# Kernel tuning notes

Measured on AMD Instinct MI355X. Metric: run time of the kernel, lower is better.

## Reference

```python
import jax, jax.numpy as jnp
import numpy as np

T, H, I, E, K, L, R = 1024, 1024, 1024, 8, 2, 4, 16
N = 2 * I  # gate_up dim


def setup_inputs() -> dict:
    key = jax.random.key(0)
    ks = jax.random.split(key, 12)
    tw = jax.random.uniform(ks[1], (T, K), dtype=jnp.float32) + 0.1
    tw = tw / tw.sum(axis=-1, keepdims=True)  # routing weights sum to 1
    return {
        "hidden_states": jax.random.normal(ks[0], (T, H), dtype=jnp.float32),
        "topk_weights": tw,
        "w13": jax.random.normal(ks[2], (E, N, H), dtype=jnp.float32) * (1.0 / np.sqrt(H)),
        "w2": jax.random.normal(ks[3], (E, H, I), dtype=jnp.float32) * (1.0 / np.sqrt(I)),
        "gate_up_lora_a": jax.random.normal(ks[4], (L, E, R, H), dtype=jnp.float32) * (1.0 / np.sqrt(H)),
        "gate_up_lora_b": jax.random.normal(ks[5], (L, E, N, R), dtype=jnp.float32) * (1.0 / np.sqrt(R)),
        "down_lora_a": jax.random.normal(ks[6], (L, E, R, I), dtype=jnp.float32) * (1.0 / np.sqrt(I)),
        "down_lora_b": jax.random.normal(ks[7], (L, E, H, R), dtype=jnp.float32) * (1.0 / np.sqrt(R)),
        "scalings": jax.random.uniform(ks[8], (L,), dtype=jnp.float32) + 0.5,
        "topk_ids": jax.random.randint(ks[9], (T, K), 0, E, dtype=jnp.int32),
        "lora_indices": jax.random.randint(ks[10], (T,), 0, L, dtype=jnp.int32),
    }


def reference(hidden_states, topk_weights, w13, w2, gate_up_lora_a,
              gate_up_lora_b, down_lora_a, down_lora_b, scalings,
              topk_ids, lora_indices):
    num_tokens, hidden = hidden_states.shape
    num_experts, gate_up_dim, _ = w13.shape
    top_k = topk_ids.shape[1]
    inter = gate_up_dim // 2
    TKp = num_tokens * top_k

    e_flat = topk_ids.reshape(-1)                      # [TK] expert per dispatched pair
    l_flat = jnp.repeat(lora_indices, top_k)           # [TK] adapter per pair
    w_flat = topk_weights.reshape(-1)                  # [TK] routing weight
    x_rep = jnp.repeat(hidden_states, top_k, axis=0)   # [TK, H]

    # ---- grouped gate_up GEMM (base path): cache1[p] = x[p] @ w13[e(p)]^T ----
    cache1 = jnp.zeros((TKp, gate_up_dim), dtype=hidden_states.dtype)
    for ei in range(num_experts):  # small fixed expert count
        mask = (e_flat == ei)[:, None]
        cache1 = cache1 + jnp.where(mask, x_rep @ w13[ei].T, 0.0)

    # ---- per-expert gate_up LoRA delta, injected BEFORE activation ----
    scal = scalings[l_flat][:, None]                   # [TK, 1]
    Ag = gate_up_lora_a[l_flat, e_flat]                # [TK, R, H]
    Bg = gate_up_lora_b[l_flat, e_flat]                # [TK, N, R]
    tmp = jnp.einsum('prh,ph->pr', Ag, x_rep)
    cache1 = cache1 + jnp.einsum('pnr,pr->pn', Bg, tmp) * scal

    # ---- silu_and_mul on (base + lora) ----
    act = jax.nn.silu(cache1[:, :inter]) * cache1[:, inter:]   # [TK, I]

    # ---- grouped down GEMM (base), routed-weight applied ----
    cache3 = jnp.zeros((TKp, hidden), dtype=hidden_states.dtype)
    for ei in range(num_experts):
        mask = (e_flat == ei)[:, None]
        cache3 = cache3 + jnp.where(mask, act @ w2[ei].T, 0.0)
    cache3 = cache3 * w_flat[:, None]

    # ---- per-expert down LoRA delta (weighted by routing weight) ----
    Ad = down_lora_a[l_flat, e_flat]                   # [TK, R, I]
    Bd = down_lora_b[l_flat, e_flat]                   # [TK, H, R]
    tmpd = jnp.einsum('pri,pi->pr', Ad, act)
    cache3 = cache3 + jnp.einsum('phr,pr->ph', Bd, tmpd) * scal * w_flat[:, None]

    # ---- combine expert outputs (moe_sum over top_k slots) ----
    return cache3.reshape(num_tokens, top_k, hidden).sum(axis=1)
```

## Files before the change

### kernel.cpp

```cpp
#include <hip/hip_runtime.h>
#include <stdint.h>

#define Td 1024
#define Hd 1024
#define Id 1024
#define Ed 8
#define Kd 2
#define Ld 4
#define Rd 16
#define Nd 2048
#define TKd (Td*Kd)

typedef __bf16 bf16x8 __attribute__((ext_vector_type(8)));
typedef float f32x4 __attribute__((ext_vector_type(4)));

__device__ __forceinline__ ushort f2bf(float f) {
    uint32_t u = __builtin_bit_cast(uint32_t, f);
    return (ushort)((u + 0x7fffu + ((u >> 16) & 1u)) >> 16);
}
__device__ __forceinline__ float bf2f(ushort u) {
    uint32_t x = ((uint32_t)u) << 16;
    return __builtin_bit_cast(float, x);
}

#define GLOAD_LDS16(g, l) __builtin_amdgcn_global_load_lds( \
    (const __attribute__((address_space(1))) uint32_t*)(const void*)(g), \
    (__attribute__((address_space(3))) uint32_t*)(void*)(l), 16, 0, 0)

#define WB 12288
#define XB 512
#define CB 384
#define TB 2048
#define ZB 1024
#define PREP_BLOCKS (WB + XB + CB + TB + ZB + 1)

__global__ __launch_bounds__(256) void k_prep(
    const float* __restrict__ hid, const float* __restrict__ w13,
    const float* __restrict__ w2, const float* __restrict__ gb,
    const float* __restrict__ db, const float* __restrict__ ga,
    const float* __restrict__ sc, const int* __restrict__ tids,
    const int* __restrict__ lidx,
    ushort* __restrict__ xb, ushort* __restrict__ w13b, ushort* __restrict__ w2b,
    ushort* __restrict__ gbbe, ushort* __restrict__ dbbe, ushort* __restrict__ tmp1e,
    float* __restrict__ out, int* __restrict__ sorted, int* __restrict__ offs)
{
    __shared__ float tr[Rd];
    __shared__ int cnt[Ed];
    __shared__ int cur[Ed];
    const int b = blockIdx.x, tid = threadIdx.x;

    if (b < WB) {
        constexpr int W138 = Ed * Nd * Hd / 8;
        int i = b * 256 + tid;
        const float* src; ushort* dst; size_t off;
        if (i < W138) { src = w13; dst = w13b; off = (size_t)i * 8; }
        else          { src = w2;  dst = w2b;  off = (size_t)(i - W138) * 8; }
        float4 a = *(const float4*)(src + off);
        float4 c = *(const float4*)(src + off + 4);
        uint4 o;
        o.x = (uint)f2bf(a.x) | ((uint)f2bf(a.y) << 16);
        o.y = (uint)f2bf(a.z) | ((uint)f2bf(a.w) << 16);
        o.z = (uint)f2bf(c.x) | ((uint)f2bf(c.y) << 16);
        o.w = (uint)f2bf(c.z) | ((uint)f2bf(c.w) << 16);
        *(uint4*)(dst + off) = o;
    } else if (b < WB + XB) {
        int i = (b - WB) * 256 + tid;
        size_t off = (size_t)i * 8;
        float4 a = *(const float4*)(hid + off);
        float4 c = *(const float4*)(hid + off + 4);
        uint4 o;
        o.x = (uint)f2bf(a.x) | ((uint)f2bf(a.y) << 16);
        o.y = (uint)f2bf(a.z) | ((uint)f2bf(a.w) << 16);
        o.z = (uint)f2bf(c.x) | ((uint)f2bf(c.y) << 16);
        o.w = (uint)f2bf(c.z) | ((uint)f2bf(c.w) << 16);
        *(uint4*)(xb + off) = o;
    } else if (b < WB + XB + CB) {
        constexpr int GR = Ld * Ed * Nd;
        int i = (b - WB - XB) * 256 + tid;
        const float* src; ushort* dst;
        if (i < GR) {
            int l = i >> 14, e = (i >> 11) & 7, n = i & 2047;
            src = gb + (size_t)i * 16;
            dst = gbbe + ((size_t)(e * Nd + n)) * 64 + l * 16;
        } else {
            int j = i - GR;
            int l = j >> 13, e = (j >> 10) & 7, n = j & 1023;
            src = db + (size_t)j * 16;
            dst = dbbe + ((size_t)(e * Id + n)) * 64 + l * 16;
        }
        float4 a0 = *(const float4*)(src);
        float4 a1 = *(const float4*)(src + 4);
        float4 a2 = *(const float4*)(src + 8);
        float4 a3 = *(const float4*)(src + 12);
        uint4 o;
        o.x = (uint)f2bf(a0.x) | ((uint)f2bf(a0.y) << 16);
        o.y = (uint)f2bf(a0.z) | ((uint)f2bf(a0.w) << 16);
        o.z = (uint)f2bf(a1.x) | ((uint)f2bf(a1.y) << 16);
        o.w = (uint)f2bf(a1.z) | ((uint)f2bf(a1.w) << 16);
        *(uint4*)(dst) = o;
        o.x = (uint)f2bf(a2.x) | ((uint)f2bf(a2.y) << 16);
        o.y = (uint)f2bf(a2.z) | ((uint)f2bf(a2.w) << 16);
        o.z = (uint)f2bf(a3.x) | ((uint)f2bf(a3.y) << 16);
        o.w = (uint)f2bf(a3.z) | ((uint)f2bf(a3.w) << 16);
        *(uint4*)(dst + 8) = o;
    } else if (b < WB + XB + CB + TB) {
        const int p = b - WB - XB - CB;
        const int e = tids[p];
        const int l = lidx[p >> 1];
        const float s = sc[l];
        const int r = tid >> 4, q = tid & 15;
        const float* A = ga + (((size_t)l * Ed + e) * Rd + r) * 1024;
        const float* x = hid + (size_t)(p >> 1) * 1024;
        float sum = 0.f;
        #pragma unroll
        for (int i = 0; i < 16; ++i) {
            int h = q * 4 + 64 * i;
            float4 a = *(const float4*)(A + h);
            float4 v = *(const float4*)(x + h);
            sum += a.x * v.x + a.y * v.y + a.z * v.z + a.w * v.w;
        }
        sum += __shfl_xor(sum, 1); sum += __shfl_xor(sum, 2);
        sum += __shfl_xor(sum, 4); sum += __shfl_xor(sum, 8);
        if (q == 0) tr[r] = sum;
        __syncthreads();
        if (tid < 32) {
            int j0 = tid * 2;
            uint v = 0;
            if ((j0 >> 4) == l)
                v = (uint)f2bf(s * tr[j0 & 15]) | ((uint)f2bf(s * tr[(j0 + 1) & 15]) << 16);
            ((uint*)(tmp1e + (size_t)p * 64))[tid] = v;
        }
    } else if (b < WB + XB + CB + TB + ZB) {
        int i = (b - WB - XB - CB - TB) * 256 + tid;
        ((float4*)out)[i] = make_float4(0.f, 0.f, 0.f, 0.f);
    } else {
        if (tid < Ed) cnt[tid] = 0;
        __syncthreads();
        int el[8];
        #pragma unroll
        for (int i = 0; i < 8; ++i) {
            el[i] = tids[tid + i * 256];
            atomicAdd(&cnt[el[i]], 1);
        }
        __syncthreads();
        if (tid == 0) {
            int s = 0;
            for (int e = 0; e < Ed; ++e) { offs[e] = s; cur[e] = s; s += cnt[e]; }
            offs[Ed] = s;
        }
        __syncthreads();
        #pragma unroll
        for (int i = 0; i < 8; ++i) {
            int pos = atomicAdd(&cur[el[i]], 1);
            sorted[pos] = tid + i * 256;
        }
    }
}

__global__ __launch_bounds__(256) void k_tmp_dn(
    const ushort* __restrict__ act, const float* __restrict__ da,
    const float* __restrict__ sc, const int* __restrict__ tids,
    const int* __restrict__ lidx, ushort* __restrict__ tmpde)
{
    const int p = blockIdx.x;
    const int e = tids[p];
    const int l = lidx[p >> 1];
    const float s = sc[l];
    const int tid = threadIdx.x;
    const int r = tid >> 4, q = tid & 15;
    const float* A = da + (((size_t)l * Ed + e) * Rd + r) * 1024;
    const ushort* x = act + (size_t)p * 1024;
    float sum = 0.f;
    #pragma unroll
    for (int i = 0; i < 8; ++i) {
        int h = q * 8 + 128 * i;
        float4 a0 = *(const float4*)(A + h);
        float4 a1 = *(const float4*)(A + h + 4);
        ushort4 v0 = *(const ushort4*)(x + h);
        ushort4 v1 = *(const ushort4*)(x + h + 4);
        sum += a0.x * bf2f(v0.x) + a0.y * bf2f(v0.y) + a0.z * bf2f(v0.z) + a0.w * bf2f(v0.w)
             + a1.x * bf2f(v1.x) + a1.y * bf2f(v1.y) + a1.z * bf2f(v1.z) + a1.w * bf2f(v1.w);
    }
    sum += __shfl_xor(sum, 1); sum += __shfl_xor(sum, 2);
    sum += __shfl_xor(sum, 4); sum += __shfl_xor(sum, 8);
    __shared__ float tr[Rd];
    if (q == 0) tr[r] = sum;
    __syncthreads();
    if (tid < 32) {
        int j0 = tid * 2;
        uint v = 0;
        if ((j0 >> 4) == l)
            v = (uint)f2bf(s * tr[j0 & 15]) | ((uint)f2bf(s * tr[(j0 + 1) & 15]) << 16);
        ((uint*)(tmpde + (size_t)p * 64))[tid] = v;
    }
}

__global__ __launch_bounds__(256) void k_gemm_gu(
    const ushort* __restrict__ xb, const ushort* __restrict__ w13b,
    const ushort* __restrict__ tmp1e, const ushort* __restrict__ gbbe,
    ushort* __restrict__ act, const int* __restrict__ sorted,
    const int* __restrict__ offs)
{
    __shared__ ushort As[128][32];
    __shared__ ushort Bs[128][32];
    const int tid = threadIdx.x, lane = tid & 63, wave = tid >> 6;
    const int wr = wave >> 1, wc = wave & 1;
    const int fr = lane & 15, fk = (lane >> 4) * 8;

    int off[Ed + 1];
    #pragma unroll
    for (int e = 0; e <= Ed; ++e) off[e] = offs[e];
    int mt[Ed]; int tot = 0;
    #pragma unroll
    for (int e = 0; e < Ed; ++e) {
        mt[e] = (off[e + 1] - off[e] + 127) / 128;
        tot += mt[e] * 16;
    }

    for (int tau = blockIdx.x; tau < tot; tau += gridDim.x) {
        int t = tau, e = 0;
        while (t >= mt[e] * 16) { t -= mt[e] * 16; ++e; }
        const int m0 = off[e] + (t >> 4) * 128;
        const int mend = off[e + 1];
        const int n0 = (t & 15) * 64;

        const ushort *asrc[2], *aesrc[2], *bsrc[2], *besrc[2];
        #pragma unroll
        for (int r = 0; r < 2; ++r) {
            int c = r * 256 + tid;
            int row = c >> 2, kc = c & 3;
            int aIdx = m0 + row; if (aIdx > mend - 1) aIdx = mend - 1;
            int p = sorted[aIdx];
            asrc[r]  = xb + (size_t)(p >> 1) * 1024 + kc * 8;
            aesrc[r] = tmp1e + (size_t)p * 64 + kc * 8;
            int grow = (row < 64) ? (n0 + row) : (1024 + n0 + row - 64);
            bsrc[r]  = w13b + ((size_t)e * Nd + grow) * 1024 + kc * 8;
            besrc[r] = gbbe + ((size_t)e * Nd + grow) * 64 + kc * 8;
        }

        f32x4 ag[4][2] = {}, au[4][2] = {};
        auto step = [&]() {
            bf16x8 af[4], bg[2], bu[2];
            #pragma unroll
            for (int mi = 0; mi < 4; ++mi)
                af[mi] = *(const bf16x8*)(&As[wr * 64 + mi * 16 + fr][fk]);
            #pragma unroll
            for (int ni = 0; ni < 2; ++ni) {
                bg[ni] = *(const bf16x8*)(&Bs[wc * 32 + ni * 16 + fr][fk]);
                bu[ni] = *(const bf16x8*)(&Bs[64 + wc * 32 + ni * 16 + fr][fk]);
            }
            #pragma unroll
            for (int mi = 0; mi < 4; ++mi)
                #pragma unroll
                for (int ni = 0; ni < 2; ++ni) {
                    ag[mi][ni] = __builtin_amdgcn_mfma_f32_16x16x32_bf16(af[mi], bg[ni], ag[mi][ni], 0, 0, 0);
                    au[mi][ni] = __builtin_amdgcn_mfma_f32_16x16x32_bf16(af[mi], bu[ni], au[mi][ni], 0, 0, 0);
                }
        };

        for (int k0 = 0; k0 < 1024; k0 += 32) {
            #pragma unroll
            for (int r = 0; r < 2; ++r) {
                GLOAD_LDS16(asrc[r] + k0, (char*)&As[0][0] + (r * 256 + wave * 64) * 16);
                GLOAD_LDS16(bsrc[r] + k0, (char*)&Bs[0][0] + (r * 256 + wave * 64) * 16);
            }
            __syncthreads();
            step();
            __syncthreads();
        }
        #pragma unroll
        for (int es = 0; es < 2; ++es) {
            #pragma unroll
            for (int r = 0; r < 2; ++r) {
                GLOAD_LDS16(aesrc[r] + es * 32, (char*)&As[0][0] + (r * 256 + wave * 64) * 16);
                GLOAD_LDS16(besrc[r] + es * 32, (char*)&Bs[0][0] + (r * 256 + wave * 64) * 16);
            }
            __syncthreads();
            step();
            __syncthreads();
        }

        const int rb = wr * 64 + (lane >> 4) * 4;
        #pragma unroll
        for (int mi = 0; mi < 4; ++mi) {
            #pragma unroll
            for (int j = 0; j < 4; ++j) {
                int sidx = m0 + rb + mi * 16 + j;
                if (sidx < mend) {
                    int p = sorted[sidx];
                    ushort* ar = act + (size_t)p * 1024 + n0 + wc * 32;
                    #pragma unroll
                    for (int ni = 0; ni < 2; ++ni) {
                        float g = ag[mi][ni][j], u = au[mi][ni][j];
                        float v = g / (1.f + __expf(-g)) * u;
                        ar[ni * 16 + fr] = f2bf(v);
                    }
                }
            }
        }
    }
}

__global__ __launch_bounds__(256) void k_gemm_dn(
    const ushort* __restrict__ act, const ushort* __restrict__ w2b,
    const ushort* __restrict__ tmpde, const ushort* __restrict__ dbbe,
    const float* __restrict__ tw, float* __restrict__ out,
    const int* __restrict__ sorted, const int* __restrict__ offs)
{
    __shared__ ushort As[128][32];
    __shared__ ushort Bs[64][32];
    const int tid = threadIdx.x, lane = tid & 63, wave = tid >> 6;
    const int wr = wave >> 1, wc = wave & 1;
    const int fr = lane & 15, fk = (lane >> 4) * 8;

    int off[Ed + 1];
    #pragma unroll
    for (int e = 0; e <= Ed; ++e) off[e] = offs[e];
    int mt[Ed]; int tot = 0;
    #pragma unroll
    for (int e = 0; e < Ed; ++e) {
        mt[e] = (off[e + 1] - off[e] + 127) / 128;
        tot += mt[e] * 16;
    }

    for (int tau = blockIdx.x; tau < tot; tau += gridDim.x) {
        int t = tau, e = 0;
        while (t >= mt[e] * 16) { t -= mt[e] * 16; ++e; }
        const int m0 = off[e] + (t >> 4) * 128;
        const int mend = off[e + 1];
        const int n0 = (t & 15) * 64;

        const ushort *asrc[2], *aesrc[2];
        #pragma unroll
        for (int r = 0; r < 2; ++r) {
            int c = r * 256 + tid;
            int row = c >> 2, kc = c & 3;
            int aIdx = m0 + row; if (aIdx > mend - 1) aIdx = mend - 1;
            int p = sorted[aIdx];
            asrc[r]  = act + (size_t)p * 1024 + kc * 8;
            aesrc[r] = tmpde + (size_t)p * 64 + kc * 8;
        }
        const ushort *bsrc, *besrc;
        {
            int row = tid >> 2, kc = tid & 3;
            bsrc  = w2b + ((size_t)e * Hd + n0 + row) * 1024 + kc * 8;
            besrc = dbbe + ((size_t)e * Hd + n0 + row) * 64 + kc * 8;
        }

        f32x4 acc[4][2] = {};
        auto step = [&]() {
            bf16x8 af[4], bv[2];
            #pragma unroll
            for (int mi = 0; mi < 4; ++mi)
                af[mi] = *(const bf16x8*)(&As[wr * 64 + mi * 16 + fr][fk]);
            #pragma unroll
            for (int ni = 0; ni < 2; ++ni)
                bv[ni] = *(const bf16x8*)(&Bs[wc * 32 + ni * 16 + fr][fk]);
            #pragma unroll
            for (int mi = 0; mi < 4; ++mi)
                #pragma unroll
                for (int ni = 0; ni < 2; ++ni)
                    acc[mi][ni] = __builtin_amdgcn_mfma_f32_16x16x32_bf16(af[mi], bv[ni], acc[mi][ni], 0, 0, 0);
        };

        for (int k0 = 0; k0 < 1024; k0 += 32) {
            #pragma unroll
            for (int r = 0; r < 2; ++r)
                GLOAD_LDS16(asrc[r] + k0, (char*)&As[0][0] + (r * 256 + wave * 64) * 16);
            GLOAD_LDS16(bsrc + k0, (char*)&Bs[0][0] + (wave * 64) * 16);
            __syncthreads();
            step();
            __syncthreads();
        }
        #pragma unroll
        for (int es = 0; es < 2; ++es) {
            #pragma unroll
            for (int r = 0; r < 2; ++r)
                GLOAD_LDS16(aesrc[r] + es * 32, (char*)&As[0][0] + (r * 256 + wave * 64) * 16);
            GLOAD_LDS16(besrc + es * 32, (char*)&Bs[0][0] + (wave * 64) * 16);
            __syncthreads();
            step();
            __syncthreads();
        }

        const int rb = wr * 64 + (lane >> 4) * 4;
        #pragma unroll
        for (int mi = 0; mi < 4; ++mi) {
            #pragma unroll
            for (int j = 0; j < 4; ++j) {
                int sidx = m0 + rb + mi * 16 + j;
                if (sidx < mend) {
                    int p = sorted[sidx];
                    float w = tw[p];
                    float* orow = out + (size_t)(p >> 1) * 1024 + n0 + wc * 32;
                    #pragma unroll
                    for (int ni = 0; ni < 2; ++ni)
                        atomicAdd(&orow[ni * 16 + fr], w * acc[mi][ni][j]);
                }
            }
        }
    }
}

extern "C" void kernel_launch(void* const* d_in, const int* in_sizes, int n_in,
                              void* d_out, int out_size, void* d_ws, size_t ws_size,
                              hipStream_t stream) {
    const float* hid  = (const float*)d_in[0];
    const float* tw   = (const float*)d_in[1];
    const float* w13  = (const float*)d_in[2];
    const float* w2   = (const float*)d_in[3];
    const float* ga   = (const float*)d_in[4];
    const float* gb   = (const float*)d_in[5];
    const float* da   = (const float*)d_in[6];
    const float* db   = (const float*)d_in[7];
    const float* sc   = (const float*)d_in[8];
    const int*   tids = (const int*)d_in[9];
    const int*   lidx = (const int*)d_in[10];
    float* out = (float*)d_out;

    char* ws = (char*)d_ws;
    ushort* xb     = (ushort*)(ws);
    ushort* w13b   = (ushort*)(ws + (2ull  << 20));
    ushort* w2b    = (ushort*)(ws + (34ull << 20));
    ushort* gbbe   = (ushort*)(ws + (50ull << 20));
    ushort* dbbe   = (ushort*)(ws + (52ull << 20));
    ushort* tmp1e  = (ushort*)(ws + (53ull << 20));
    ushort* tmpde  = (ushort*)(ws + (53ull << 20) + (256u << 10));
    ushort* act    = (ushort*)(ws + (54ull << 20));
    int*    sorted = (int*)(ws + (58ull << 20));
    int*    offs   = (int*)(ws + (58ull << 20) + TKd * 4);

    k_prep<<<PREP_BLOCKS, 256, 0, stream>>>(hid, w13, w2, gb, db, ga, sc, tids, lidx,
                                            xb, w13b, w2b, gbbe, dbbe, tmp1e,
                                            out, sorted, offs);
    k_gemm_gu<<<512, 256, 0, stream>>>(xb, w13b, tmp1e, gbbe, act, sorted, offs);
    k_tmp_dn<<<TKd, 256, 0, stream>>>(act, da, sc, tids, lidx, tmpde);
    k_gemm_dn<<<512, 256, 0, stream>>>(act, w2b, tmpde, dbbe, tw, out, sorted, offs);
}
```

Measured before the change: 107.2 us.

## Convert fp32 expert weights to bf16 inside GEMMs with double-buffered LDS

Drops the separate prep pass that converted w13 and w2 to bf16 in the workspace. The GEMM kernels now load the fp32 weights directly into registers, convert them to bf16 and store them into a second LDS buffer while MFMAs run on the current one. This removes a full read and write of the weight tensors and adds software pipelining of the K loop. The cost is fp32 weight reads inside the GEMM, which doubles B-operand traffic per tile and repeats it across the M tiles of each expert, plus doubled LDS usage.

```diff
diff --git a/kernel.cpp b/kernel.cpp
--- a/kernel.cpp
+++ b/kernel.cpp
@@ -22,49 +22,39 @@
     uint32_t x = ((uint32_t)u) << 16;
     return __builtin_bit_cast(float, x);
 }
+__device__ __forceinline__ bf16x8 pack8(float4 a, float4 b) {
+    bf16x8 r;
+    r[0] = (__bf16)a.x; r[1] = (__bf16)a.y; r[2] = (__bf16)a.z; r[3] = (__bf16)a.w;
+    r[4] = (__bf16)b.x; r[5] = (__bf16)b.y; r[6] = (__bf16)b.z; r[7] = (__bf16)b.w;
+    return r;
+}
 
 #define GLOAD_LDS16(g, l) __builtin_amdgcn_global_load_lds( \
     (const __attribute__((address_space(1))) uint32_t*)(const void*)(g), \
     (__attribute__((address_space(3))) uint32_t*)(void*)(l), 16, 0, 0)
 
-#define WB 12288
 #define XB 512
 #define CB 384
 #define TB 2048
 #define ZB 1024
-#define PREP_BLOCKS (WB + XB + CB + TB + ZB + 1)
+#define PREP_BLOCKS (XB + CB + TB + ZB + 1)
 
 __global__ __launch_bounds__(256) void k_prep(
-    const float* __restrict__ hid, const float* __restrict__ w13,
-    const float* __restrict__ w2, const float* __restrict__ gb,
+    const float* __restrict__ hid, const float* __restrict__ gb,
     const float* __restrict__ db, const float* __restrict__ ga,
     const float* __restrict__ sc, const int* __restrict__ tids,
     const int* __restrict__ lidx,
-    ushort* __restrict__ xb, ushort* __restrict__ w13b, ushort* __restrict__ w2b,
-    ushort* __restrict__ gbbe, ushort* __restrict__ dbbe, ushort* __restrict__ tmp1e,
-    float* __restrict__ out, int* __restrict__ sorted, int* __restrict__ offs)
+    ushort* __restrict__ xb, ushort* __restrict__ gbbe, ushort* __restrict__ dbbe,
+    ushort* __restrict__ tmp1e, float* __restrict__ out,
+    int* __restrict__ sorted, int* __restrict__ offs)
 {
     __shared__ float tr[Rd];
     __shared__ int cnt[Ed];
     __shared__ int cur[Ed];
     const int b = blockIdx.x, tid = threadIdx.x;
 
-    if (b < WB) {
-        constexpr int W138 = Ed * Nd * Hd / 8;
+    if (b < XB) {
         int i = b * 256 + tid;
-        const float* src; ushort* dst; size_t off;
-        if (i < W138) { src = w13; dst = w13b; off = (size_t)i * 8; }
-        else          { src = w2;  dst = w2b;  off = (size_t)(i - W138) * 8; }
-        float4 a = *(const float4*)(src + off);
-        float4 c = *(const float4*)(src + off + 4);
-        uint4 o;
-        o.x = (uint)f2bf(a.x) | ((uint)f2bf(a.y) << 16);
-        o.y = (uint)f2bf(a.z) | ((uint)f2bf(a.w) << 16);
-        o.z = (uint)f2bf(c.x) | ((uint)f2bf(c.y) << 16);
-        o.w = (uint)f2bf(c.z) | ((uint)f2bf(c.w) << 16);
-        *(uint4*)(dst + off) = o;
-    } else if (b < WB + XB) {
-        int i = (b - WB) * 256 + tid;
         size_t off = (size_t)i * 8;
         float4 a = *(const float4*)(hid + off);
         float4 c = *(const float4*)(hid + off + 4);
@@ -74,9 +64,9 @@
         o.z = (uint)f2bf(c.x) | ((uint)f2bf(c.y) << 16);
         o.w = (uint)f2bf(c.z) | ((uint)f2bf(c.w) << 16);
         *(uint4*)(xb + off) = o;
-    } else if (b < WB + XB + CB) {
+    } else if (b < XB + CB) {
         constexpr int GR = Ld * Ed * Nd;
-        int i = (b - WB - XB) * 256 + tid;
+        int i = (b - XB) * 256 + tid;
         const float* src; ushort* dst;
         if (i < GR) {
             int l = i >> 14, e = (i >> 11) & 7, n = i & 2047;
@@ -103,8 +93,8 @@
         o.z = (uint)f2bf(a3.x) | ((uint)f2bf(a3.y) << 16);
         o.w = (uint)f2bf(a3.z) | ((uint)f2bf(a3.w) << 16);
         *(uint4*)(dst + 8) = o;
-    } else if (b < WB + XB + CB + TB) {
-        const int p = b - WB - XB - CB;
+    } else if (b < XB + CB + TB) {
+        const int p = b - XB - CB;
         const int e = tids[p];
         const int l = lidx[p >> 1];
         const float s = sc[l];
@@ -130,8 +120,8 @@
                 v = (uint)f2bf(s * tr[j0 & 15]) | ((uint)f2bf(s * tr[(j0 + 1) & 15]) << 16);
             ((uint*)(tmp1e + (size_t)p * 64))[tid] = v;
         }
-    } else if (b < WB + XB + CB + TB + ZB) {
-        int i = (b - WB - XB - CB - TB) * 256 + tid;
+    } else if (b < XB + CB + TB + ZB) {
+        int i = (b - XB - CB - TB) * 256 + tid;
         ((float4*)out)[i] = make_float4(0.f, 0.f, 0.f, 0.f);
     } else {
         if (tid < Ed) cnt[tid] = 0;
@@ -196,13 +186,13 @@
 }
 
 __global__ __launch_bounds__(256) void k_gemm_gu(
-    const ushort* __restrict__ xb, const ushort* __restrict__ w13b,
+    const ushort* __restrict__ xb, const float* __restrict__ w13,
     const ushort* __restrict__ tmp1e, const ushort* __restrict__ gbbe,
     ushort* __restrict__ act, const int* __restrict__ sorted,
     const int* __restrict__ offs)
 {
-    __shared__ ushort As[128][32];
-    __shared__ ushort Bs[128][32];
+    __shared__ ushort As[2][128][32];
+    __shared__ ushort Bs[2][128][32];
     const int tid = threadIdx.x, lane = tid & 63, wave = tid >> 6;
     const int wr = wave >> 1, wc = wave & 1;
     const int fr = lane & 15, fk = (lane >> 4) * 8;
@@ -224,7 +214,7 @@
         const int mend = off[e + 1];
         const int n0 = (t & 15) * 64;
 
-        const ushort *asrc[2], *aesrc[2], *bsrc[2], *besrc[2];
+        const ushort *asrc[2], *aesrc[2], *besrc[2];
         #pragma unroll
         for (int r = 0; r < 2; ++r) {
             int c = r * 256 + tid;
@@ -234,20 +224,22 @@
             asrc[r]  = xb + (size_t)(p >> 1) * 1024 + kc * 8;
             aesrc[r] = tmp1e + (size_t)p * 64 + kc * 8;
             int grow = (row < 64) ? (n0 + row) : (1024 + n0 + row - 64);
-            bsrc[r]  = w13b + ((size_t)e * Nd + grow) * 1024 + kc * 8;
             besrc[r] = gbbe + ((size_t)e * Nd + grow) * 64 + kc * 8;
         }
+        const int brow = tid >> 1, bhalf = tid & 1;
+        const int bg_row = (brow < 64) ? (n0 + brow) : (1024 + n0 + brow - 64);
+        const float* bsrc = w13 + ((size_t)e * Nd + bg_row) * 1024 + bhalf * 16;
 
         f32x4 ag[4][2] = {}, au[4][2] = {};
-        auto step = [&]() {
+        auto step = [&](int buf) {
             bf16x8 af[4], bg[2], bu[2];
             #pragma unroll
             for (int mi = 0; mi < 4; ++mi)
-                af[mi] = *(const bf16x8*)(&As[wr * 64 + mi * 16 + fr][fk]);
+                af[mi] = *(const bf16x8*)(&As[buf][wr * 64 + mi * 16 + fr][fk]);
             #pragma unroll
             for (int ni = 0; ni < 2; ++ni) {
-                bg[ni] = *(const bf16x8*)(&Bs[wc * 32 + ni * 16 + fr][fk]);
-                bu[ni] = *(const bf16x8*)(&Bs[64 + wc * 32 + ni * 16 + fr][fk]);
+                bg[ni] = *(const bf16x8*)(&Bs[buf][wc * 32 + ni * 16 + fr][fk]);
+                bu[ni] = *(const bf16x8*)(&Bs[buf][64 + wc * 32 + ni * 16 + fr][fk]);
             }
             #pragma unroll
             for (int mi = 0; mi < 4; ++mi)
@@ -258,26 +250,47 @@
                 }
         };
 
-        for (int k0 = 0; k0 < 1024; k0 += 32) {
+        #pragma unroll
+        for (int r = 0; r < 2; ++r)
+            GLOAD_LDS16(asrc[r], (char*)&As[0][0][0] + (r * 256 + wave * 64) * 16);
+        {
+            float4 y0 = *(const float4*)(bsrc);
+            float4 y1 = *(const float4*)(bsrc + 4);
+            float4 y2 = *(const float4*)(bsrc + 8);
+            float4 y3 = *(const float4*)(bsrc + 12);
+            *(bf16x8*)(&Bs[0][brow][bhalf * 16])     = pack8(y0, y1);
+            *(bf16x8*)(&Bs[0][brow][bhalf * 16 + 8]) = pack8(y2, y3);
+        }
+        __syncthreads();
+
+        int buf = 0;
+        for (int k0 = 32; k0 < 1024; k0 += 32) {
+            #pragma unroll
+            for (int r = 0; r < 2; ++r)
+                GLOAD_LDS16(asrc[r] + k0, (char*)&As[buf ^ 1][0][0] + (r * 256 + wave * 64) * 16);
+            float4 y0 = *(const float4*)(bsrc + k0);
+            float4 y1 = *(const float4*)(bsrc + k0 + 4);
+            float4 y2 = *(const float4*)(bsrc + k0 + 8);
+            float4 y3 = *(const float4*)(bsrc + k0 + 12);
+
+            step(buf);
+
+            *(bf16x8*)(&Bs[buf ^ 1][brow][bhalf * 16])     = pack8(y0, y1);
+            *(bf16x8*)(&Bs[buf ^ 1][brow][bhalf * 16 + 8]) = pack8(y2, y3);
+            __syncthreads();
+            buf ^= 1;
+        }
+        step(buf);
+
+        #pragma unroll
+        for (int es = 0; es < 2; ++es) {
             #pragma unroll
             for (int r = 0; r < 2; ++r) {
-                GLOAD_LDS16(asrc[r] + k0, (char*)&As[0][0] + (r * 256 + wave * 64) * 16);
-                GLOAD_LDS16(bsrc[r] + k0, (char*)&Bs[0][0] + (r * 256 + wave * 64) * 16);
+                GLOAD_LDS16(aesrc[r] + es * 32, (char*)&As[es][0][0] + (r * 256 + wave * 64) * 16);
+                GLOAD_LDS16(besrc[r] + es * 32, (char*)&Bs[es][0][0] + (r * 256 + wave * 64) * 16);
             }
             __syncthreads();
-            step();
-            __syncthreads();
-        }
-        #pragma unroll
-        for (int es = 0; es < 2; ++es) {
-            #pragma unroll
-            for (int r = 0; r < 2; ++r) {
-                GLOAD_LDS16(aesrc[r] + es * 32, (char*)&As[0][0] + (r * 256 + wave * 64) * 16);
-                GLOAD_LDS16(besrc[r] + es * 32, (char*)&Bs[0][0] + (r * 256 + wave * 64) * 16);
-            }
-            __syncthreads();
-            step();
-            __syncthreads();
+            step(es);
         }
 
         const int rb = wr * 64 + (lane >> 4) * 4;
@@ -298,17 +311,18 @@
                 }
             }
         }
+        __syncthreads();
     }
 }
 
 __global__ __launch_bounds__(256) void k_gemm_dn(
-    const ushort* __restrict__ act, const ushort* __restrict__ w2b,
+    const ushort* __restrict__ act, const float* __restrict__ w2,
     const ushort* __restrict__ tmpde, const ushort* __restrict__ dbbe,
     const float* __restrict__ tw, float* __restrict__ out,
     const int* __restrict__ sorted, const int* __restrict__ offs)
 {
-    __shared__ ushort As[128][32];
-    __shared__ ushort Bs[64][32];
+    __shared__ ushort As[2][128][32];
+    __shared__ ushort Bs[2][64][32];
     const int tid = threadIdx.x, lane = tid & 63, wave = tid >> 6;
     const int wr = wave >> 1, wc = wave & 1;
     const int fr = lane & 15, fk = (lane >> 4) * 8;
@@ -330,7 +344,7 @@
         const int mend = off[e + 1];
         const int n0 = (t & 15) * 64;
 
-        const ushort *asrc[2], *aesrc[2];
+        const ushort *asrc[2], *aesrc[2], *besrc;
         #pragma unroll
         for (int r = 0; r < 2; ++r) {
             int c = r * 256 + tid;
@@ -340,22 +354,19 @@
             asrc[r]  = act + (size_t)p * 1024 + kc * 8;
             aesrc[r] = tmpde + (size_t)p * 64 + kc * 8;
         }
-        const ushort *bsrc, *besrc;
-        {
-            int row = tid >> 2, kc = tid & 3;
-            bsrc  = w2b + ((size_t)e * Hd + n0 + row) * 1024 + kc * 8;
-            besrc = dbbe + ((size_t)e * Hd + n0 + row) * 64 + kc * 8;
-        }
+        besrc = dbbe + ((size_t)e * Hd + n0 + (tid >> 2)) * 64 + (tid & 3) * 8;
+        const int brow = tid >> 2, bq = tid & 3;
+        const float* bsrc = w2 + ((size_t)e * Hd + n0 + brow) * 1024 + bq * 8;
 
         f32x4 acc[4][2] = {};
-        auto step = [&]() {
+        auto step = [&](int buf) {
             bf16x8 af[4], bv[2];
             #pragma unroll
             for (int mi = 0; mi < 4; ++mi)
-                af[mi] = *(const bf16x8*)(&As[wr * 64 + mi * 16 + fr][fk]);
+                af[mi] = *(const bf16x8*)(&As[buf][wr * 64 + mi * 16 + fr][fk]);
             #pragma unroll
             for (int ni = 0; ni < 2; ++ni)
-                bv[ni] = *(const bf16x8*)(&Bs[wc * 32 + ni * 16 + fr][fk]);
+                bv[ni] = *(const bf16x8*)(&Bs[buf][wc * 32 + ni * 16 + fr][fk]);
             #pragma unroll
             for (int mi = 0; mi < 4; ++mi)
                 #pragma unroll
@@ -363,24 +374,40 @@
                     acc[mi][ni] = __builtin_amdgcn_mfma_f32_16x16x32_bf16(af[mi], bv[ni], acc[mi][ni], 0, 0, 0);
         };
 
-        for (int k0 = 0; k0 < 1024; k0 += 32) {
+        #pragma unroll
+        for (int r = 0; r < 2; ++r)
+            GLOAD_LDS16(asrc[r], (char*)&As[0][0][0] + (r * 256 + wave * 64) * 16);
+        {
+            float4 y0 = *(const float4*)(bsrc);
+            float4 y1 = *(const float4*)(bsrc + 4);
+            *(bf16x8*)(&Bs[0][brow][bq * 8]) = pack8(y0, y1);
+        }
+        __syncthreads();
+
+        int buf = 0;
+        for (int k0 = 32; k0 < 1024; k0 += 32) {
             #pragma unroll
             for (int r = 0; r < 2; ++r)
-                GLOAD_LDS16(asrc[r] + k0, (char*)&As[0][0] + (r * 256 + wave * 64) * 16);
-            GLOAD_LDS16(bsrc + k0, (char*)&Bs[0][0] + (wave * 64) * 16);
+                GLOAD_LDS16(asrc[r] + k0, (char*)&As[buf ^ 1][0][0] + (r * 256 + wave * 64) * 16);
+            float4 y0 = *(const float4*)(bsrc + k0);
+            float4 y1 = *(const float4*)(bsrc + k0 + 4);
+
+            step(buf);
+
+            *(bf16x8*)(&Bs[buf ^ 1][brow][bq * 8]) = pack8(y0, y1);
             __syncthreads();
-            step();
+            buf ^= 1;
+        }
+        step(buf);
+
+        #pragma unroll
+        for (int es = 0; es < 2; ++es) {
+            #pragma unroll
+            for (int r = 0; r < 2; ++r)
+                GLOAD_LDS16(aesrc[r] + es * 32, (char*)&As[es][0][0] + (r * 256 + wave * 64) * 16);
+            GLOAD_LDS16(besrc + es * 32, (char*)&Bs[es][0][0] + (wave * 64) * 16);
             __syncthreads();
-        }
-        #pragma unroll
-        for (int es = 0; es < 2; ++es) {
-            #pragma unroll
-            for (int r = 0; r < 2; ++r)
-                GLOAD_LDS16(aesrc[r] + es * 32, (char*)&As[0][0] + (r * 256 + wave * 64) * 16);
-            GLOAD_LDS16(besrc + es * 32, (char*)&Bs[0][0] + (wave * 64) * 16);
-            __syncthreads();
-            step();
-            __syncthreads();
+            step(es);
         }
 
         const int rb = wr * 64 + (lane >> 4) * 4;
@@ -399,6 +426,7 @@
                 }
             }
         }
+        __syncthreads();
     }
 }
 
@@ -420,20 +448,17 @@
 
     char* ws = (char*)d_ws;
     ushort* xb     = (ushort*)(ws);
-    ushort* w13b   = (ushort*)(ws + (2ull  << 20));
-    ushort* w2b    = (ushort*)(ws + (34ull << 20));
-    ushort* gbbe   = (ushort*)(ws + (50ull << 20));
-    ushort* dbbe   = (ushort*)(ws + (52ull << 20));
-    ushort* tmp1e  = (ushort*)(ws + (53ull << 20));
-    ushort* tmpde  = (ushort*)(ws + (53ull << 20) + (256u << 10));
-    ushort* act    = (ushort*)(ws + (54ull << 20));
-    int*    sorted = (int*)(ws + (58ull << 20));
-    int*    offs   = (int*)(ws + (58ull << 20) + TKd * 4);
-
-    k_prep<<<PREP_BLOCKS, 256, 0, stream>>>(hid, w13, w2, gb, db, ga, sc, tids, lidx,
-                                            xb, w13b, w2b, gbbe, dbbe, tmp1e,
-                                            out, sorted, offs);
-    k_gemm_gu<<<512, 256, 0, stream>>>(xb, w13b, tmp1e, gbbe, act, sorted, offs);
+    ushort* gbbe   = (ushort*)(ws + (2ull << 20));
+    ushort* dbbe   = (ushort*)(ws + (4ull << 20));
+    ushort* tmp1e  = (ushort*)(ws + (5ull << 20));
+    ushort* tmpde  = (ushort*)(ws + (5ull << 20) + (256u << 10));
+    ushort* act    = (ushort*)(ws + (6ull << 20));
+    int*    sorted = (int*)(ws + (10ull << 20));
+    int*    offs   = (int*)(ws + (10ull << 20) + TKd * 4);
+
+    k_prep<<<PREP_BLOCKS, 256, 0, stream>>>(hid, gb, db, ga, sc, tids, lidx,
+                                            xb, gbbe, dbbe, tmp1e, out, sorted, offs);
+    k_gemm_gu<<<512, 256, 0, stream>>>(xb, w13, tmp1e, gbbe, act, sorted, offs);
     k_tmp_dn<<<TKd, 256, 0, stream>>>(act, da, sc, tids, lidx, tmpde);
-    k_gemm_dn<<<512, 256, 0, stream>>>(act, w2b, tmpde, dbbe, tw, out, sorted, offs);
-}
+    k_gemm_dn<<<512, 256, 0, stream>>>(act, w2, tmpde, dbbe, tw, out, sorted, offs);
+}
```

Measured after the change: 100.8 us. -6.0%, faster.

## Move w2 bf16 conversion into gate-up GEMM launch and widen prep conversion

Applied to the files above, without the earlier changes.

The w2 fp32-to-bf16 conversion moves out of the prep kernel and into extra blocks appended to the gate-up GEMM launch, so it can overlap with GEMM work instead of sitting on the critical path of prep. The remaining conversions now handle 16 elements per thread instead of 8, which halves the block count. The block order in prep is also changed so the LoRA-A dot-product blocks are scheduled earlier. The GEMM loop stride is fixed at the GEMM block count. The extra conversion blocks compete with the GEMM blocks for bandwidth and CUs, and they may be scheduled after the GEMM tiles rather than alongside them.

```diff
diff --git a/kernel.cpp b/kernel.cpp
--- a/kernel.cpp
+++ b/kernel.cpp
@@ -22,25 +22,41 @@
     uint32_t x = ((uint32_t)u) << 16;
     return __builtin_bit_cast(float, x);
 }
+__device__ __forceinline__ void cvt16(const float* __restrict__ s, ushort* __restrict__ d) {
+    float4 a0 = *(const float4*)(s);
+    float4 a1 = *(const float4*)(s + 4);
+    float4 a2 = *(const float4*)(s + 8);
+    float4 a3 = *(const float4*)(s + 12);
+    uint4 o0, o1;
+    o0.x = (uint)f2bf(a0.x) | ((uint)f2bf(a0.y) << 16);
+    o0.y = (uint)f2bf(a0.z) | ((uint)f2bf(a0.w) << 16);
+    o0.z = (uint)f2bf(a1.x) | ((uint)f2bf(a1.y) << 16);
+    o0.w = (uint)f2bf(a1.z) | ((uint)f2bf(a1.w) << 16);
+    o1.x = (uint)f2bf(a2.x) | ((uint)f2bf(a2.y) << 16);
+    o1.y = (uint)f2bf(a2.z) | ((uint)f2bf(a2.w) << 16);
+    o1.z = (uint)f2bf(a3.x) | ((uint)f2bf(a3.y) << 16);
+    o1.w = (uint)f2bf(a3.z) | ((uint)f2bf(a3.w) << 16);
+    *(uint4*)(d) = o0;
+    *(uint4*)(d + 8) = o1;
+}
 
 #define GLOAD_LDS16(g, l) __builtin_amdgcn_global_load_lds( \
     (const __attribute__((address_space(1))) uint32_t*)(const void*)(g), \
     (__attribute__((address_space(3))) uint32_t*)(void*)(l), 16, 0, 0)
 
-#define WB 12288
-#define XB 512
+#define W13C 4096
+#define TB 2048
+#define XB 256
 #define CB 384
-#define TB 2048
 #define ZB 1024
-#define PREP_BLOCKS (WB + XB + CB + TB + ZB + 1)
+#define PREP_BLOCKS (W13C + TB + XB + CB + ZB + 1)
 
 __global__ __launch_bounds__(256) void k_prep(
     const float* __restrict__ hid, const float* __restrict__ w13,
-    const float* __restrict__ w2, const float* __restrict__ gb,
-    const float* __restrict__ db, const float* __restrict__ ga,
-    const float* __restrict__ sc, const int* __restrict__ tids,
-    const int* __restrict__ lidx,
-    ushort* __restrict__ xb, ushort* __restrict__ w13b, ushort* __restrict__ w2b,
+    const float* __restrict__ gb, const float* __restrict__ db,
+    const float* __restrict__ ga, const float* __restrict__ sc,
+    const int* __restrict__ tids, const int* __restrict__ lidx,
+    ushort* __restrict__ xb, ushort* __restrict__ w13b,
     ushort* __restrict__ gbbe, ushort* __restrict__ dbbe, ushort* __restrict__ tmp1e,
     float* __restrict__ out, int* __restrict__ sorted, int* __restrict__ offs)
 {
@@ -49,34 +65,42 @@
     __shared__ int cur[Ed];
     const int b = blockIdx.x, tid = threadIdx.x;
 
-    if (b < WB) {
-        constexpr int W138 = Ed * Nd * Hd / 8;
-        int i = b * 256 + tid;
-        const float* src; ushort* dst; size_t off;
-        if (i < W138) { src = w13; dst = w13b; off = (size_t)i * 8; }
-        else          { src = w2;  dst = w2b;  off = (size_t)(i - W138) * 8; }
-        float4 a = *(const float4*)(src + off);
-        float4 c = *(const float4*)(src + off + 4);
-        uint4 o;
-        o.x = (uint)f2bf(a.x) | ((uint)f2bf(a.y) << 16);
-        o.y = (uint)f2bf(a.z) | ((uint)f2bf(a.w) << 16);
-        o.z = (uint)f2bf(c.x) | ((uint)f2bf(c.y) << 16);
-        o.w = (uint)f2bf(c.z) | ((uint)f2bf(c.w) << 16);
-        *(uint4*)(dst + off) = o;
-    } else if (b < WB + XB) {
-        int i = (b - WB) * 256 + tid;
-        size_t off = (size_t)i * 8;
-        float4 a = *(const float4*)(hid + off);
-        float4 c = *(const float4*)(hid + off + 4);
-        uint4 o;
-        o.x = (uint)f2bf(a.x) | ((uint)f2bf(a.y) << 16);
-        o.y = (uint)f2bf(a.z) | ((uint)f2bf(a.w) << 16);
-        o.z = (uint)f2bf(c.x) | ((uint)f2bf(c.y) << 16);
-        o.w = (uint)f2bf(c.z) | ((uint)f2bf(c.w) << 16);
-        *(uint4*)(xb + off) = o;
-    } else if (b < WB + XB + CB) {
+    if (b < W13C) {
+        size_t off = ((size_t)b * 256 + tid) * 16;
+        cvt16(w13 + off, w13b + off);
+    } else if (b < W13C + TB) {
+        const int p = b - W13C;
+        const int e = tids[p];
+        const int l = lidx[p >> 1];
+        const float s = sc[l];
+        const int r = tid >> 4, q = tid & 15;
+        const float* A = ga + (((size_t)l * Ed + e) * Rd + r) * 1024;
+        const float* x = hid + (size_t)(p >> 1) * 1024;
+        float sum = 0.f;
+        #pragma unroll
+        for (int i = 0; i < 16; ++i) {
+            int h = q * 4 + 64 * i;
+            float4 a = *(const float4*)(A + h);
+            float4 v = *(const float4*)(x + h);
+            sum += a.x * v.x + a.y * v.y + a.z * v.z + a.w * v.w;
+        }
+        sum += __shfl_xor(sum, 1); sum += __shfl_xor(sum, 2);
+        sum += __shfl_xor(sum, 4); sum += __shfl_xor(sum, 8);
+        if (q == 0) tr[r] = sum;
+        __syncthreads();
+        if (tid < 32) {
+            int j0 = tid * 2;
+            uint v = 0;
+            if ((j0 >> 4) == l)
+                v = (uint)f2bf(s * tr[j0 & 15]) | ((uint)f2bf(s * tr[(j0 + 1) & 15]) << 16);
+            ((uint*)(tmp1e + (size_t)p * 64))[tid] = v;
+        }
+    } else if (b < W13C + TB + XB) {
+        size_t off = ((size_t)(b - W13C - TB) * 256 + tid) * 16;
+        cvt16(hid + off, xb + off);
+    } else if (b < W13C + TB + XB + CB) {
         constexpr int GR = Ld * Ed * Nd;
-        int i = (b - WB - XB) * 256 + tid;
+        int i = (b - W13C - TB - XB) * 256 + tid;
         const float* src; ushort* dst;
         if (i < GR) {
             int l = i >> 14, e = (i >> 11) & 7, n = i & 2047;
@@ -88,50 +112,9 @@
             src = db + (size_t)j * 16;
             dst = dbbe + ((size_t)(e * Id + n)) * 64 + l * 16;
         }
-        float4 a0 = *(const float4*)(src);
-        float4 a1 = *(const float4*)(src + 4);
-        float4 a2 = *(const float4*)(src + 8);
-        float4 a3 = *(const float4*)(src + 12);
-        uint4 o;
-        o.x = (uint)f2bf(a0.x) | ((uint)f2bf(a0.y) << 16);
-        o.y = (uint)f2bf(a0.z) | ((uint)f2bf(a0.w) << 16);
-        o.z = (uint)f2bf(a1.x) | ((uint)f2bf(a1.y) << 16);
-        o.w = (uint)f2bf(a1.z) | ((uint)f2bf(a1.w) << 16);
-        *(uint4*)(dst) = o;
-        o.x = (uint)f2bf(a2.x) | ((uint)f2bf(a2.y) << 16);
-        o.y = (uint)f2bf(a2.z) | ((uint)f2bf(a2.w) << 16);
-        o.z = (uint)f2bf(a3.x) | ((uint)f2bf(a3.y) << 16);
-        o.w = (uint)f2bf(a3.z) | ((uint)f2bf(a3.w) << 16);
-        *(uint4*)(dst + 8) = o;
-    } else if (b < WB + XB + CB + TB) {
-        const int p = b - WB - XB - CB;
-        const int e = tids[p];
-        const int l = lidx[p >> 1];
-        const float s = sc[l];
-        const int r = tid >> 4, q = tid & 15;
-        const float* A = ga + (((size_t)l * Ed + e) * Rd + r) * 1024;
-        const float* x = hid + (size_t)(p >> 1) * 1024;
-        float sum = 0.f;
-        #pragma unroll
-        for (int i = 0; i < 16; ++i) {
-            int h = q * 4 + 64 * i;
-            float4 a = *(const float4*)(A + h);
-            float4 v = *(const float4*)(x + h);
-            sum += a.x * v.x + a.y * v.y + a.z * v.z + a.w * v.w;
-        }
-        sum += __shfl_xor(sum, 1); sum += __shfl_xor(sum, 2);
-        sum += __shfl_xor(sum, 4); sum += __shfl_xor(sum, 8);
-        if (q == 0) tr[r] = sum;
-        __syncthreads();
-        if (tid < 32) {
-            int j0 = tid * 2;
-            uint v = 0;
-            if ((j0 >> 4) == l)
-                v = (uint)f2bf(s * tr[j0 & 15]) | ((uint)f2bf(s * tr[(j0 + 1) & 15]) << 16);
-            ((uint*)(tmp1e + (size_t)p * 64))[tid] = v;
-        }
-    } else if (b < WB + XB + CB + TB + ZB) {
-        int i = (b - WB - XB - CB - TB) * 256 + tid;
+        cvt16(src, dst);
+    } else if (b < W13C + TB + XB + CB + ZB) {
+        int i = (b - W13C - TB - XB - CB) * 256 + tid;
         ((float4*)out)[i] = make_float4(0.f, 0.f, 0.f, 0.f);
     } else {
         if (tid < Ed) cnt[tid] = 0;
@@ -195,15 +178,27 @@
     }
 }
 
+#define GUB 512
+#define W2C 2048
+
 __global__ __launch_bounds__(256) void k_gemm_gu(
     const ushort* __restrict__ xb, const ushort* __restrict__ w13b,
     const ushort* __restrict__ tmp1e, const ushort* __restrict__ gbbe,
+    const float* __restrict__ w2, ushort* __restrict__ w2b,
     ushort* __restrict__ act, const int* __restrict__ sorted,
     const int* __restrict__ offs)
 {
     __shared__ ushort As[128][32];
     __shared__ ushort Bs[128][32];
-    const int tid = threadIdx.x, lane = tid & 63, wave = tid >> 6;
+    const int tid = threadIdx.x;
+
+    if (blockIdx.x >= GUB) {
+        size_t off = ((size_t)(blockIdx.x - GUB) * 256 + tid) * 16;
+        cvt16(w2 + off, w2b + off);
+        return;
+    }
+
+    const int lane = tid & 63, wave = tid >> 6;
     const int wr = wave >> 1, wc = wave & 1;
     const int fr = lane & 15, fk = (lane >> 4) * 8;
 
@@ -217,7 +212,7 @@
         tot += mt[e] * 16;
     }
 
-    for (int tau = blockIdx.x; tau < tot; tau += gridDim.x) {
+    for (int tau = blockIdx.x; tau < tot; tau += GUB) {
         int t = tau, e = 0;
         while (t >= mt[e] * 16) { t -= mt[e] * 16; ++e; }
         const int m0 = off[e] + (t >> 4) * 128;
@@ -430,10 +425,9 @@
     int*    sorted = (int*)(ws + (58ull << 20));
     int*    offs   = (int*)(ws + (58ull << 20) + TKd * 4);
 
-    k_prep<<<PREP_BLOCKS, 256, 0, stream>>>(hid, w13, w2, gb, db, ga, sc, tids, lidx,
-                                            xb, w13b, w2b, gbbe, dbbe, tmp1e,
-                                            out, sorted, offs);
-    k_gemm_gu<<<512, 256, 0, stream>>>(xb, w13b, tmp1e, gbbe, act, sorted, offs);
+    k_prep<<<PREP_BLOCKS, 256, 0, stream>>>(hid, w13, gb, db, ga, sc, tids, lidx,
+                                            xb, w13b, gbbe, dbbe, tmp1e, out, sorted, offs);
+    k_gemm_gu<<<GUB + W2C, 256, 0, stream>>>(xb, w13b, tmp1e, gbbe, w2, w2b, act, sorted, offs);
     k_tmp_dn<<<TKd, 256, 0, stream>>>(act, da, sc, tids, lidx, tmpde);
     k_gemm_dn<<<512, 256, 0, stream>>>(act, w2b, tmpde, dbbe, tw, out, sorted, offs);
 }
```

Measured after the change: 103.1 us. 1.04x faster.
